# Kernel optimization log

Measured on AMD Instinct MI355X. Metric: run time of the kernel, lower is better.

The kernel has to match this reference:

```python
import jax, jax.numpy as jnp
import numpy as np

N, M = 8192, 128  # n samples, m features


def setup_inputs() -> dict:
    key = jax.random.key(0)
    k0, k1, k2, k3, k4 = jax.random.split(key, 5)
    L = jax.random.normal(k0, (N, M), dtype=jnp.float32)
    X = jax.random.normal(k1, (N, M), dtype=jnp.float32)
    Y = jax.random.normal(k2, (N,), dtype=jnp.float32)
    # params of the sub-network `net` (modeled as Linear(m, m))
    Wnet = jax.random.normal(k3, (M, M), dtype=jnp.float32) / np.float32(np.sqrt(M))
    bnet = jax.random.normal(k4, (M,), dtype=jnp.float32) * 0.01
    return {"L": L, "X": X, "Y": Y, "Wnet": Wnet, "bnet": bnet}


def reference(L, X, Y, Wnet, bnet):
    # A[i] = L[i] * X[i];  B[j] = net(X[j]) * X[j]   (elementwise feature weighting)
    A = L * X                                    # [n, m]
    B = (X @ Wnet + bnet) * X                    # [n, m] -- net(X[j]) computed once, batched
    # pairwise L2 distances: dist[i,j] = ||A_i - B_j||
    d2 = (jnp.sum(A * A, axis=1)[:, None]
          + jnp.sum(B * B, axis=1)[None, :]
          - 2.0 * (A @ B.T))                     # [n, n]
    dist = jnp.sqrt(jnp.maximum(d2, 1e-12))
    drum = jnp.exp(-dist)                        # [n, n] kernel weights
    # Nadaraya-Watson prediction: pred_i = (drum_i . Y) / sum_j drum_ij
    pred = (drum @ Y) / jnp.sum(drum, axis=1)    # [n]
    return jnp.sum((Y - pred) ** 2)              # scalar loss
```

## Files before the change

kernel.cpp:

```cpp
#include <hip/hip_runtime.h>
#include <hip/hip_bf16.h>
#include <cstdint>


#define N_ 8192
#define M_ 128
#define SQRT2K2_ 2.0402789f

typedef __bf16 bf16x8 __attribute__((ext_vector_type(8)));
typedef float  f32x4  __attribute__((ext_vector_type(4)));

__device__ __forceinline__ unsigned short f2bf(float f) {
    unsigned int x = __float_as_uint(f);
    unsigned int r = x + 0x7fffu + ((x >> 16) & 1u);
    return (unsigned short)(r >> 16);
}


__global__ __launch_bounds__(256) void prep_kernel(
    const float* __restrict__ L, const float* __restrict__ X,
    const float* __restrict__ Y, const float* __restrict__ Wnet,
    const float* __restrict__ bnet,
    unsigned short* __restrict__ Asw, unsigned short* __restrict__ Bsw,
    float* __restrict__ naS, float2* __restrict__ nbY,
    float* __restrict__ sumw, float* __restrict__ sumwy,
    float* __restrict__ out)
{
    __shared__ float Ws[128 * 128];
    __shared__ float Xs[16][128];
    const int tid  = threadIdx.x;
    const int row0 = blockIdx.x * 16;
    const int k4   = tid & 31;
    const int rr   = tid >> 5;

    #pragma unroll
    for (int i = 0; i < 16; ++i)
        ((float4*)Ws)[tid + i * 256] = ((const float4*)Wnet)[tid + i * 256];
    #pragma unroll
    for (int i = 0; i < 2; ++i)
        ((float4*)Xs)[tid + i * 256] =
            ((const float4*)(X + (size_t)row0 * 128))[tid + i * 256];
    __syncthreads();

    float acc0[4] = {0.f, 0.f, 0.f, 0.f};
    float acc1[4] = {0.f, 0.f, 0.f, 0.f};
    const int r0 = rr * 2, r1 = rr * 2 + 1;
    #pragma unroll 2
    for (int c4 = 0; c4 < 128; c4 += 4) {
        const float4 x0 = *(const float4*)&Xs[r0][c4];
        const float4 x1 = *(const float4*)&Xs[r1][c4];
        const float4 wc0 = *(const float4*)&Ws[(c4 + 0) * 128 + k4 * 4];
        const float4 wc1 = *(const float4*)&Ws[(c4 + 1) * 128 + k4 * 4];
        const float4 wc2 = *(const float4*)&Ws[(c4 + 2) * 128 + k4 * 4];
        const float4 wc3 = *(const float4*)&Ws[(c4 + 3) * 128 + k4 * 4];
        const float x0e[4] = {x0.x, x0.y, x0.z, x0.w};
        const float x1e[4] = {x1.x, x1.y, x1.z, x1.w};
        const float4 wce[4] = {wc0, wc1, wc2, wc3};
        #pragma unroll
        for (int c = 0; c < 4; ++c) {
            acc0[0] = fmaf(x0e[c], wce[c].x, acc0[0]);
            acc0[1] = fmaf(x0e[c], wce[c].y, acc0[1]);
            acc0[2] = fmaf(x0e[c], wce[c].z, acc0[2]);
            acc0[3] = fmaf(x0e[c], wce[c].w, acc0[3]);
            acc1[0] = fmaf(x1e[c], wce[c].x, acc1[0]);
            acc1[1] = fmaf(x1e[c], wce[c].y, acc1[1]);
            acc1[2] = fmaf(x1e[c], wce[c].z, acc1[2]);
            acc1[3] = fmaf(x1e[c], wce[c].w, acc1[3]);
        }
    }

    const float4 bn4 = *(const float4*)(bnet + k4 * 4);
    float napart[2], nbpart[2];
    #pragma unroll
    for (int j = 0; j < 2; ++j) {
        const int ln  = rr * 2 + j;
        const int row = row0 + ln;
        const float* acc = j ? acc1 : acc0;
        const float4 xv = *(const float4*)(&Xs[ln][k4 * 4]);
        const float4 l4 = *(const float4*)(L + (size_t)row * 128 + k4 * 4);
        unsigned short apk[4], bpk[4];
        float nA_ = 0.f, nB_ = 0.f;
        const float xe[4] = {xv.x, xv.y, xv.z, xv.w};
        const float le[4] = {l4.x, l4.y, l4.z, l4.w};
        const float be[4] = {bn4.x, bn4.y, bn4.z, bn4.w};
        #pragma unroll
        for (int e = 0; e < 4; ++e) {
            float a = le[e] * xe[e] * SQRT2K2_;
            float b = (acc[e] + be[e]) * xe[e] * SQRT2K2_;
            unsigned short ua = f2bf(a), ub = f2bf(b);
            apk[e] = ua; bpk[e] = ub;
            float af = __uint_as_float((unsigned)ua << 16);
            float bf = __uint_as_float((unsigned)ub << 16);
            nA_ = fmaf(af, af, nA_);
            nB_ = fmaf(bf, bf, nB_);
        }
        napart[j] = nA_; nbpart[j] = nB_;
        size_t off = (size_t)blockIdx.x * 2048 + (size_t)(k4 >> 3) * 512
                   + (size_t)((k4 >> 1) & 3) * 128 + (size_t)ln * 8 + (k4 & 1) * 4;
        uint2 pa = make_uint2((unsigned)apk[0] | ((unsigned)apk[1] << 16),
                              (unsigned)apk[2] | ((unsigned)apk[3] << 16));
        uint2 pb = make_uint2((unsigned)bpk[0] | ((unsigned)bpk[1] << 16),
                              (unsigned)bpk[2] | ((unsigned)bpk[3] << 16));
        *(uint2*)(Asw + off) = pa;
        *(uint2*)(Bsw + off) = pb;
    }

    #pragma unroll
    for (int m = 1; m <= 16; m <<= 1) {
        napart[0] += __shfl_xor(napart[0], m, 64);
        napart[1] += __shfl_xor(napart[1], m, 64);
        nbpart[0] += __shfl_xor(nbpart[0], m, 64);
        nbpart[1] += __shfl_xor(nbpart[1], m, 64);
    }
    if (k4 == 0) {
        #pragma unroll
        for (int j = 0; j < 2; ++j) {
            int row = row0 + rr * 2 + j;
            naS[row] = -0.5f * napart[j];
            nbY[row] = make_float2(-0.5f * nbpart[j], Y[row]);
        }
    }
    if (tid < 16) sumw[row0 + tid] = 0.f;
    else if (tid < 32) sumwy[row0 + tid - 16] = 0.f;
    if (blockIdx.x == 0 && tid == 32) out[0] = 0.f;
}

__global__ __launch_bounds__(256, 2) void pairwise_kernel(
    const unsigned short* __restrict__ Asw, const unsigned short* __restrict__ Bsw,
    const float* __restrict__ naS, const float2* __restrict__ nbY,
    float* __restrict__ sumw, float* __restrict__ sumwy)
{
    const int tid  = threadIdx.x;
    const int wv   = tid >> 6;
    const int lane = tid & 63;
    const int ln16 = lane & 15;
    const int quad = lane >> 4;
    const int i0   = blockIdx.x * 256;
    const int j0   = blockIdx.y * 512;

    bf16x8 afrag[4][4];
    float  nna[4][4];
    #pragma unroll
    for (int rt = 0; rt < 4; ++rt) {
        const int gA = (i0 >> 4) + wv * 4 + rt;
        const unsigned short* ap = Asw + (size_t)gA * 2048 + lane * 8;
        #pragma unroll
        for (int ks = 0; ks < 4; ++ks)
            afrag[rt][ks] = *(const bf16x8*)(ap + ks * 512);
        #pragma unroll
        for (int r = 0; r < 4; ++r)
            nna[rt][r] = naS[gA * 16 + quad * 4 + r];
    }

    float accw[4][4], accwy[4][4];
    #pragma unroll
    for (int rt = 0; rt < 4; ++rt)
        #pragma unroll
        for (int r = 0; r < 4; ++r) { accw[rt][r] = 0.f; accwy[rt][r] = 0.f; }

    const unsigned short* bbase = Bsw + (size_t)(j0 >> 4) * 2048 + lane * 8;
    const float2* nbbase = nbY + j0 + ln16;

    #pragma unroll 2
    for (int ct = 0; ct < 32; ++ct) {
        const unsigned short* bp = bbase + (size_t)ct * 2048;
        bf16x8 bfrag[4];
        #pragma unroll
        for (int ks = 0; ks < 4; ++ks)
            bfrag[ks] = *(const bf16x8*)(bp + ks * 512);
        const float2 nv = nbbase[ct * 16];

        #pragma unroll
        for (int rt = 0; rt < 4; ++rt) {
            f32x4 s;
            #pragma unroll
            for (int r = 0; r < 4; ++r) s[r] = nna[rt][r] + nv.x;
            #pragma unroll
            for (int ks = 0; ks < 4; ++ks)
                s = __builtin_amdgcn_mfma_f32_16x16x32_bf16(
                        afrag[rt][ks], bfrag[ks], s, 0, 0, 0);
            #pragma unroll
            for (int r = 0; r < 4; ++r) {
                float w = __builtin_amdgcn_exp2f(
                              -__builtin_amdgcn_sqrtf(__builtin_fabsf(s[r])));
                accw[rt][r] += w;
                accwy[rt][r] = fmaf(w, nv.y, accwy[rt][r]);
            }
        }
    }

    #pragma unroll
    for (int rt = 0; rt < 4; ++rt)
        #pragma unroll
        for (int r = 0; r < 4; ++r) {
            float w  = accw[rt][r];
            float wy = accwy[rt][r];
            #pragma unroll
            for (int m = 1; m <= 8; m <<= 1) {
                w  += __shfl_xor(w,  m, 64);
                wy += __shfl_xor(wy, m, 64);
            }
            if (ln16 == 0) {
                int row = i0 + wv * 64 + rt * 16 + quad * 4 + r;
                atomicAdd(&sumw[row],  w);
                atomicAdd(&sumwy[row], wy);
            }
        }
}

__global__ __launch_bounds__(256) void finish_kernel(
    const float* __restrict__ Y, const float* __restrict__ sumw,
    const float* __restrict__ sumwy, float* __restrict__ out)
{
    __shared__ float red[4];
    const int tid = threadIdx.x;
    const int idx = blockIdx.x * 256 + tid;
    float4 w4  = ((const float4*)sumw)[idx];
    float4 wy4 = ((const float4*)sumwy)[idx];
    float4 y4  = ((const float4*)Y)[idx];
    const float we[4]  = {w4.x, w4.y, w4.z, w4.w};
    const float wye[4] = {wy4.x, wy4.y, wy4.z, wy4.w};
    const float ye[4]  = {y4.x, y4.y, y4.z, y4.w};
    float acc = 0.f;
    #pragma unroll
    for (int e = 0; e < 4; ++e) {
        float pred = wye[e] * __builtin_amdgcn_rcpf(we[e]);
        float d = ye[e] - pred;
        acc = fmaf(d, d, acc);
    }
    #pragma unroll
    for (int m = 1; m < 64; m <<= 1) acc += __shfl_xor(acc, m, 64);
    if ((tid & 63) == 0) red[tid >> 6] = acc;
    __syncthreads();
    if (tid == 0) {
        float v = red[0] + red[1] + red[2] + red[3];
        atomicAdd(out, v);
    }
}

extern "C" void kernel_launch(void* const* d_in, const int* in_sizes, int n_in,
                              void* d_out, int out_size, void* d_ws, size_t ws_size,
                              hipStream_t stream)
{
    const float* L    = (const float*)d_in[0];
    const float* X    = (const float*)d_in[1];
    const float* Y    = (const float*)d_in[2];
    const float* Wnet = (const float*)d_in[3];
    const float* bnet = (const float*)d_in[4];
    float* out = (float*)d_out;

    char* ws = (char*)d_ws;
    unsigned short* Asw = (unsigned short*)(ws);
    unsigned short* Bsw = (unsigned short*)(ws + (size_t)2 * 1024 * 1024);
    float*  naS   = (float*) (ws + (size_t)4 * 1024 * 1024);
    float2* nbYp  = (float2*)(ws + (size_t)4 * 1024 * 1024 + 32 * 1024);
    float*  sumw  = (float*) (ws + (size_t)4 * 1024 * 1024 + 96 * 1024);
    float*  sumwy = (float*) (ws + (size_t)4 * 1024 * 1024 + 128 * 1024);

    prep_kernel<<<N_ / 16, 256, 0, stream>>>(L, X, Y, Wnet, bnet,
                                             Asw, Bsw, naS, nbYp, sumw, sumwy, out);
    pairwise_kernel<<<dim3(N_ / 256, 16), 256, 0, stream>>>(Asw, Bsw, naS, nbYp,
                                                            sumw, sumwy);
    finish_kernel<<<8, 256, 0, stream>>>(Y, sumw, sumwy, out);
}
```

Baseline: 102.8 us.

## Compute net(X) in prep kernel with bf16 MFMA instead of LDS FP32 FMAs

The prep kernel is rewritten so each wave handles 16 rows and computes X@Wnet with bf16 16x16x32 MFMA instructions. Weight fragments are converted on the fly from global memory, so the 64KB shared-memory copy of Wnet per block goes away. The grid shrinks from N/16 to N/64 blocks. In exchange the net output is computed from bf16-rounded X and W, which loses some precision, and the weight reads are strided global loads.

```diff
diff --git a/kernel.cpp b/kernel.cpp
--- a/kernel.cpp
+++ b/kernel.cpp
@@ -9,6 +9,7 @@
 
 typedef __bf16 bf16x8 __attribute__((ext_vector_type(8)));
 typedef float  f32x4  __attribute__((ext_vector_type(4)));
+typedef unsigned int u32;
 
 __device__ __forceinline__ unsigned short f2bf(float f) {
     unsigned int x = __float_as_uint(f);
@@ -26,103 +27,91 @@
     float* __restrict__ sumw, float* __restrict__ sumwy,
     float* __restrict__ out)
 {
-    __shared__ float Ws[128 * 128];
-    __shared__ float Xs[16][128];
     const int tid  = threadIdx.x;
-    const int row0 = blockIdx.x * 16;
-    const int k4   = tid & 31;
-    const int rr   = tid >> 5;
-
-    #pragma unroll
-    for (int i = 0; i < 16; ++i)
-        ((float4*)Ws)[tid + i * 256] = ((const float4*)Wnet)[tid + i * 256];
-    #pragma unroll
-    for (int i = 0; i < 2; ++i)
-        ((float4*)Xs)[tid + i * 256] =
-            ((const float4*)(X + (size_t)row0 * 128))[tid + i * 256];
-    __syncthreads();
-
-    float acc0[4] = {0.f, 0.f, 0.f, 0.f};
-    float acc1[4] = {0.f, 0.f, 0.f, 0.f};
-    const int r0 = rr * 2, r1 = rr * 2 + 1;
-    #pragma unroll 2
-    for (int c4 = 0; c4 < 128; c4 += 4) {
-        const float4 x0 = *(const float4*)&Xs[r0][c4];
-        const float4 x1 = *(const float4*)&Xs[r1][c4];
-        const float4 wc0 = *(const float4*)&Ws[(c4 + 0) * 128 + k4 * 4];
-        const float4 wc1 = *(const float4*)&Ws[(c4 + 1) * 128 + k4 * 4];
-        const float4 wc2 = *(const float4*)&Ws[(c4 + 2) * 128 + k4 * 4];
-        const float4 wc3 = *(const float4*)&Ws[(c4 + 3) * 128 + k4 * 4];
-        const float x0e[4] = {x0.x, x0.y, x0.z, x0.w};
-        const float x1e[4] = {x1.x, x1.y, x1.z, x1.w};
-        const float4 wce[4] = {wc0, wc1, wc2, wc3};
-        #pragma unroll
-        for (int c = 0; c < 4; ++c) {
-            acc0[0] = fmaf(x0e[c], wce[c].x, acc0[0]);
-            acc0[1] = fmaf(x0e[c], wce[c].y, acc0[1]);
-            acc0[2] = fmaf(x0e[c], wce[c].z, acc0[2]);
-            acc0[3] = fmaf(x0e[c], wce[c].w, acc0[3]);
-            acc1[0] = fmaf(x1e[c], wce[c].x, acc1[0]);
-            acc1[1] = fmaf(x1e[c], wce[c].y, acc1[1]);
-            acc1[2] = fmaf(x1e[c], wce[c].z, acc1[2]);
-            acc1[3] = fmaf(x1e[c], wce[c].w, acc1[3]);
-        }
-    }
-
-    const float4 bn4 = *(const float4*)(bnet + k4 * 4);
-    float napart[2], nbpart[2];
-    #pragma unroll
-    for (int j = 0; j < 2; ++j) {
-        const int ln  = rr * 2 + j;
-        const int row = row0 + ln;
-        const float* acc = j ? acc1 : acc0;
-        const float4 xv = *(const float4*)(&Xs[ln][k4 * 4]);
-        const float4 l4 = *(const float4*)(L + (size_t)row * 128 + k4 * 4);
-        unsigned short apk[4], bpk[4];
-        float nA_ = 0.f, nB_ = 0.f;
-        const float xe[4] = {xv.x, xv.y, xv.z, xv.w};
-        const float le[4] = {l4.x, l4.y, l4.z, l4.w};
-        const float be[4] = {bn4.x, bn4.y, bn4.z, bn4.w};
-        #pragma unroll
-        for (int e = 0; e < 4; ++e) {
+    const int wv   = tid >> 6;
+    const int lane = tid & 63;
+    const int ln16 = lane & 15;
+    const int quad = lane >> 4;
+    const int g    = blockIdx.x * 4 + wv;
+    const int j    = g * 16 + ln16;
+
+    bf16x8 xfrag[4];
+    float na_part = 0.f;
+    #pragma unroll
+    for (int ks = 0; ks < 4; ++ks) {
+        const int k0 = quad * 8 + ks * 32;
+        const float4 xlo = *(const float4*)(X + (size_t)j * 128 + k0);
+        const float4 xhi = *(const float4*)(X + (size_t)j * 128 + k0 + 4);
+        const float4 llo = *(const float4*)(L + (size_t)j * 128 + k0);
+        const float4 lhi = *(const float4*)(L + (size_t)j * 128 + k0 + 4);
+        const float xe[8] = {xlo.x, xlo.y, xlo.z, xlo.w, xhi.x, xhi.y, xhi.z, xhi.w};
+        const float le[8] = {llo.x, llo.y, llo.z, llo.w, lhi.x, lhi.y, lhi.z, lhi.w};
+        unsigned short xp[8], ap[8];
+        #pragma unroll
+        for (int e = 0; e < 8; ++e) {
+            xp[e] = f2bf(xe[e]);
             float a = le[e] * xe[e] * SQRT2K2_;
-            float b = (acc[e] + be[e]) * xe[e] * SQRT2K2_;
-            unsigned short ua = f2bf(a), ub = f2bf(b);
-            apk[e] = ua; bpk[e] = ub;
-            float af = __uint_as_float((unsigned)ua << 16);
-            float bf = __uint_as_float((unsigned)ub << 16);
-            nA_ = fmaf(af, af, nA_);
-            nB_ = fmaf(bf, bf, nB_);
-        }
-        napart[j] = nA_; nbpart[j] = nB_;
-        size_t off = (size_t)blockIdx.x * 2048 + (size_t)(k4 >> 3) * 512
-                   + (size_t)((k4 >> 1) & 3) * 128 + (size_t)ln * 8 + (k4 & 1) * 4;
-        uint2 pa = make_uint2((unsigned)apk[0] | ((unsigned)apk[1] << 16),
-                              (unsigned)apk[2] | ((unsigned)apk[3] << 16));
-        uint2 pb = make_uint2((unsigned)bpk[0] | ((unsigned)bpk[1] << 16),
-                              (unsigned)bpk[2] | ((unsigned)bpk[3] << 16));
-        *(uint2*)(Asw + off) = pa;
-        *(uint2*)(Bsw + off) = pb;
-    }
-
-    #pragma unroll
-    for (int m = 1; m <= 16; m <<= 1) {
-        napart[0] += __shfl_xor(napart[0], m, 64);
-        napart[1] += __shfl_xor(napart[1], m, 64);
-        nbpart[0] += __shfl_xor(nbpart[0], m, 64);
-        nbpart[1] += __shfl_xor(nbpart[1], m, 64);
-    }
-    if (k4 == 0) {
-        #pragma unroll
-        for (int j = 0; j < 2; ++j) {
-            int row = row0 + rr * 2 + j;
-            naS[row] = -0.5f * napart[j];
-            nbY[row] = make_float2(-0.5f * nbpart[j], Y[row]);
-        }
-    }
-    if (tid < 16) sumw[row0 + tid] = 0.f;
-    else if (tid < 32) sumwy[row0 + tid - 16] = 0.f;
-    if (blockIdx.x == 0 && tid == 32) out[0] = 0.f;
+            unsigned short ua = f2bf(a);
+            ap[e] = ua;
+            float af = __uint_as_float((u32)ua << 16);
+            na_part = fmaf(af, af, na_part);
+        }
+        uint4 xi = make_uint4(xp[0] | ((u32)xp[1] << 16), xp[2] | ((u32)xp[3] << 16),
+                              xp[4] | ((u32)xp[5] << 16), xp[6] | ((u32)xp[7] << 16));
+        xfrag[ks] = *(bf16x8*)&xi;
+        uint4 ai = make_uint4(ap[0] | ((u32)ap[1] << 16), ap[2] | ((u32)ap[3] << 16),
+                              ap[4] | ((u32)ap[5] << 16), ap[6] | ((u32)ap[7] << 16));
+        *(uint4*)(Asw + (size_t)g * 2048 + (size_t)ks * 512 + (size_t)lane * 8) = ai;
+    }
+    na_part += __shfl_xor(na_part, 16, 64);
+    na_part += __shfl_xor(na_part, 32, 64);
+    if (lane < 16) naS[j] = -0.5f * na_part;
+
+    float nb_part = 0.f;
+    #pragma unroll
+    for (int ct = 0; ct < 8; ++ct) {
+        const int cb = ct * 16 + quad * 4;
+        const int c  = ct * 16 + ln16;
+        const float4 bn = *(const float4*)(bnet + cb);
+        f32x4 s;
+        s[0] = bn.x; s[1] = bn.y; s[2] = bn.z; s[3] = bn.w;
+        #pragma unroll
+        for (int ks = 0; ks < 4; ++ks) {
+            unsigned short wp[8];
+            #pragma unroll
+            for (int e = 0; e < 8; ++e) {
+                const int k = quad * 8 + e + ks * 32;
+                wp[e] = f2bf(Wnet[(size_t)k * 128 + c]);
+            }
+            uint4 wi = make_uint4(wp[0] | ((u32)wp[1] << 16), wp[2] | ((u32)wp[3] << 16),
+                                  wp[4] | ((u32)wp[5] << 16), wp[6] | ((u32)wp[7] << 16));
+            bf16x8 wfrag = *(bf16x8*)&wi;
+            s = __builtin_amdgcn_mfma_f32_16x16x32_bf16(wfrag, xfrag[ks], s, 0, 0, 0);
+        }
+        const float4 xv = *(const float4*)(X + (size_t)j * 128 + cb);
+        const float xe2[4] = {xv.x, xv.y, xv.z, xv.w};
+        unsigned short bp[4];
+        #pragma unroll
+        for (int r = 0; r < 4; ++r) {
+            float b = s[r] * xe2[r] * SQRT2K2_;
+            unsigned short ub = f2bf(b);
+            bp[r] = ub;
+            float bf_ = __uint_as_float((u32)ub << 16);
+            nb_part = fmaf(bf_, bf_, nb_part);
+        }
+        size_t off = (size_t)g * 2048 + (size_t)(cb >> 5) * 512
+                   + (size_t)((cb >> 3) & 3) * 128 + (size_t)ln16 * 8 + (cb & 7);
+        *(uint2*)(Bsw + off) = make_uint2(bp[0] | ((u32)bp[1] << 16),
+                                          bp[2] | ((u32)bp[3] << 16));
+    }
+    nb_part += __shfl_xor(nb_part, 16, 64);
+    nb_part += __shfl_xor(nb_part, 32, 64);
+    if (lane < 16) nbY[j] = make_float2(-0.5f * nb_part, Y[j]);
+
+    const int z0 = blockIdx.x * 64;
+    if (tid < 64) sumw[z0 + tid] = 0.f;
+    else if (tid < 128) sumwy[z0 + tid - 64] = 0.f;
+    if (blockIdx.x == 0 && tid == 128) out[0] = 0.f;
 }
 
 __global__ __launch_bounds__(256, 2) void pairwise_kernel(
@@ -257,7 +246,7 @@
     float*  sumw  = (float*) (ws + (size_t)4 * 1024 * 1024 + 96 * 1024);
     float*  sumwy = (float*) (ws + (size_t)4 * 1024 * 1024 + 128 * 1024);
 
-    prep_kernel<<<N_ / 16, 256, 0, stream>>>(L, X, Y, Wnet, bnet,
+    prep_kernel<<<N_ / 64, 256, 0, stream>>>(L, X, Y, Wnet, bnet,
                                              Asw, Bsw, naS, nbYp, sumw, sumwy, out);
     pairwise_kernel<<<dim3(N_ / 256, 16), 256, 0, stream>>>(Asw, Bsw, naS, nbYp,
                                                             sumw, sumwy);
```

Measured after the change: 110.0 us. +7.0%, slower.
